# Performance work log

Measured on AMD Instinct MI355X. Metric: run time of the kernel, lower is better.

## Reference

```python
import jax, jax.numpy as jnp
import numpy as np

H = 8              # n_heads
N_PER_GRAPH = 64   # nodes per graph (equal-sized graphs)


def setup_inputs() -> dict:
    key = jax.random.key(0)
    ks = jax.random.split(key, 5)
    total, D = 65536, 512
    x = jax.random.normal(ks[0], (total, D), dtype=jnp.float32)
    batch = jnp.arange(total, dtype=jnp.int64) // N_PER_GRAPH  # sorted graph ids
    s = 1.0 / np.sqrt(D).astype(np.float32)
    # nn.MultiheadAttention packed in-proj (xavier-ish uniform) + zero bias
    in_proj_w = jax.random.uniform(ks[1], (3 * D, D), jnp.float32, -s, s)
    in_proj_b = jnp.zeros((3 * D,), jnp.float32)
    out_proj_w = jax.random.uniform(ks[2], (D, D), jnp.float32, -s, s)
    out_proj_b = jnp.zeros((D,), jnp.float32)
    gate_w = jax.random.uniform(ks[3], (1, D), jnp.float32, -s, s)
    gate_b = jnp.zeros((1,), jnp.float32)
    return {"x": x, "batch": batch, "in_proj_w": in_proj_w, "in_proj_b": in_proj_b,
            "out_proj_w": out_proj_w, "out_proj_b": out_proj_b,
            "gate_w": gate_w, "gate_b": gate_b}


def reference(x, batch, in_proj_w, in_proj_b, out_proj_w, out_proj_b, gate_w, gate_b):
    total, D = x.shape
    G = total // N_PER_GRAPH
    hd = D // H
    xg = x.reshape(G, N_PER_GRAPH, D)                       # [G, N, D]
    # packed qkv projection (torch: x @ in_proj_w.T + in_proj_b)
    qkv = jnp.einsum('gnd,ed->gne', xg, in_proj_w) + in_proj_b
    q, k, v = jnp.split(qkv, 3, axis=-1)
    def to_heads(t):
        return t.reshape(G, N_PER_GRAPH, H, hd).transpose(0, 2, 1, 3)  # [G, H, N, hd]
    q, k, v = to_heads(q), to_heads(k), to_heads(v)
    scores = jnp.einsum('ghnd,ghmd->ghnm', q, k) * (1.0 / np.sqrt(hd))
    attn = jax.nn.softmax(scores, axis=-1)
    ctx = jnp.einsum('ghnm,ghmd->ghnd', attn, v)
    ctx = ctx.transpose(0, 2, 1, 3).reshape(G, N_PER_GRAPH, D)
    attn_out = jnp.einsum('gnd,ed->gne', ctx, out_proj_w) + out_proj_b  # [G, N, D]
    gates = jax.nn.sigmoid(jnp.einsum('gnd,od->gno', attn_out, gate_w) + gate_b)
    return (attn_out * gates).sum(axis=1)                   # [G, D]
```

## Files before the change

kernel.cpp:

```cpp
#include <hip/hip_runtime.h>
#include <stdint.h>


typedef __attribute__((ext_vector_type(8))) short short8;
typedef __attribute__((ext_vector_type(4))) float f32x4;

#define D_ 512

#define WQKV_OFF   0u
#define WO_OFF     1572864u
#define UPART_OFF  2097152u
#define U_OFF      2129920u
#define C0_OFF     2131968u
#define SG_OFF     2132032u
#define WCTX_OFF   2136128u

__device__ __forceinline__ unsigned short f2bf(float f) {
    union { float f; unsigned int u; } t; t.f = f;
    unsigned int u = t.u;
    return (unsigned short)((u + 0x7FFFu + ((u >> 16) & 1u)) >> 16);
}
__device__ __forceinline__ unsigned pack2(float a, float b) {
    return (unsigned)f2bf(a) | ((unsigned)f2bf(b) << 16);
}

__global__ __launch_bounds__(256)
void convert_weights(const float* __restrict__ wqkv, const float* __restrict__ wo,
                     unsigned short* __restrict__ wbf) {
    const int i4 = blockIdx.x * 256 + threadIdx.x;
    float4 v;
    if (i4 < 196608) v = *(const float4*)(wqkv + (size_t)i4 * 4);
    else             v = *(const float4*)(wo   + (size_t)(i4 - 196608) * 4);
    uint2 p; p.x = pack2(v.x, v.y); p.y = pack2(v.z, v.w);
    *(uint2*)(wbf + (size_t)i4 * 4) = p;
}

__global__ __launch_bounds__(256)
void compute_u_partial(const float* __restrict__ wo, const float* __restrict__ gw,
                       float* __restrict__ upart) {
    const int b = blockIdx.x;
    const int t = threadIdx.x;
    float a0 = 0.f, a1 = 0.f;
    #pragma unroll 4
    for (int e = b * 32; e < b * 32 + 32; ++e) {
        const float ge = gw[e];
        a0 += wo[(size_t)e * 512 + t]       * ge;
        a1 += wo[(size_t)e * 512 + t + 256] * ge;
    }
    upart[b * 512 + t] = a0; upart[b * 512 + t + 256] = a1;
}

__global__ __launch_bounds__(256)
void finalize_u(const float* __restrict__ upart, const float* __restrict__ bo,
                const float* __restrict__ gw, const float* __restrict__ gb,
                float* __restrict__ u, float* __restrict__ c0) {
    const int t = threadIdx.x;
    float s0 = 0.f, s1 = 0.f;
    #pragma unroll
    for (int b = 0; b < 16; ++b) { s0 += upart[b*512 + t]; s1 += upart[b*512 + t + 256]; }
    u[t] = s0; u[t + 256] = s1;
    __shared__ float rb[256];
    rb[t] = bo[t] * gw[t] + bo[t + 256] * gw[t + 256];
    __syncthreads();
    for (int s = 128; s > 0; s >>= 1) { if (t < s) rb[t] += rb[t + s]; __syncthreads(); }
    if (t == 0) c0[0] = rb[0] + gb[0];
}

union U8 { unsigned u[4]; short8 s; };

__global__ __launch_bounds__(512, 2)
void attn_ctx_kernel(const float* __restrict__ x,
                     const unsigned short* __restrict__ wqkv,
                     const float* __restrict__ bqkv,
                     const float* __restrict__ u,
                     const float* __restrict__ c0,
                     unsigned short* __restrict__ wctx_ws,
                     float* __restrict__ sumgate)
{
    __shared__ unsigned short xs[64][520];
    __shared__ unsigned short scr[8][64][72];
    __shared__ float logitp[8][64];
    __shared__ float gatev[64];

    const int g    = blockIdx.x;
    const int tid  = threadIdx.x;
    const int w    = tid >> 6;
    const int lane = tid & 63;
    const int l15  = lane & 15;
    const int quad = lane >> 4;

    #pragma unroll
    for (int i = 0; i < 16; ++i) {
        int idx = tid + i * 512;
        int row = idx >> 7;
        int c4  = idx & 127;
        float4 v = *(const float4*)(x + ((size_t)(g*64 + row))*512 + c4*4);
        uint2 p; p.x = pack2(v.x, v.y); p.y = pack2(v.z, v.w);
        *(uint2*)(&xs[row][c4*4]) = p;
    }
    __syncthreads();

    const int h = w;
    unsigned short (*S)[72] = scr[w];

    U8 qA[4][2], kB[4][2];
    #pragma unroll
    for (int dt = 0; dt < 4; ++dt) {
        f32x4 aq[4], ak[4], av[4];
        #pragma unroll
        for (int nt = 0; nt < 4; ++nt) {
            aq[nt] = (f32x4){0.f,0.f,0.f,0.f};
            ak[nt] = (f32x4){0.f,0.f,0.f,0.f};
            av[nt] = (f32x4){0.f,0.f,0.f,0.f};
        }
        const unsigned short* wq = wqkv + (size_t)(          h*64 + dt*16 + l15) * 512;
        const unsigned short* wk = wqkv + (size_t)( 512 +    h*64 + dt*16 + l15) * 512;
        const unsigned short* wv = wqkv + (size_t)(1024 +    h*64 + dt*16 + l15) * 512;
        #pragma unroll 4
        for (int ks = 0; ks < 16; ++ks) {
            const int col = ks*32 + quad*8;
            short8 a0 = *(const short8*)(wq + col);
            short8 a1 = *(const short8*)(wk + col);
            short8 a2 = *(const short8*)(wv + col);
            #pragma unroll
            for (int nt = 0; nt < 4; ++nt) {
                short8 b = *(const short8*)(&xs[nt*16 + l15][col]);
                aq[nt] = __builtin_amdgcn_mfma_f32_16x16x32_bf16(a0, b, aq[nt], 0,0,0);
                ak[nt] = __builtin_amdgcn_mfma_f32_16x16x32_bf16(a1, b, ak[nt], 0,0,0);
                av[nt] = __builtin_amdgcn_mfma_f32_16x16x32_bf16(a2, b, av[nt], 0,0,0);
            }
        }
        float bq[4], bk2[4], bv2[4];
        #pragma unroll
        for (int r = 0; r < 4; ++r) {
            bq[r]  = bqkv[          h*64 + dt*16 + quad*4 + r];
            bk2[r] = bqkv[ 512 +    h*64 + dt*16 + quad*4 + r];
            bv2[r] = bqkv[1024 +    h*64 + dt*16 + quad*4 + r];
        }
        const bool take = ((quad >> 1) == (dt & 1));
        const int  ks2  = dt >> 1;
        #pragma unroll
        for (int nt = 0; nt < 4; ++nt) {
            unsigned q01 = pack2(aq[nt][0]+bq[0],  aq[nt][1]+bq[1]);
            unsigned q23 = pack2(aq[nt][2]+bq[2],  aq[nt][3]+bq[3]);
            unsigned k01 = pack2(ak[nt][0]+bk2[0], ak[nt][1]+bk2[1]);
            unsigned k23 = pack2(ak[nt][2]+bk2[2], ak[nt][3]+bk2[3]);
            #pragma unroll
            for (int j = 0; j < 4; ++j) {
                int srcl = ((quad & 1)*2 + (j >> 1))*16 + l15;
                unsigned tq = (unsigned)__shfl((int)((j & 1) ? q23 : q01), srcl);
                unsigned tk = (unsigned)__shfl((int)((j & 1) ? k23 : k01), srcl);
                if (take) { qA[nt][ks2].u[j] = tq; kB[nt][ks2].u[j] = tk; }
            }
            #pragma unroll
            for (int r = 0; r < 4; ++r)
                S[dt*16 + quad*4 + r][nt*16 + l15] = f2bf(av[nt][r] + bv2[r]);
        }
    }

    f32x4 sacc[4][4];
    #pragma unroll
    for (int a = 0; a < 4; ++a)
        #pragma unroll
        for (int b = 0; b < 4; ++b) sacc[a][b] = (f32x4){0.f,0.f,0.f,0.f};
    #pragma unroll
    for (int ks2 = 0; ks2 < 2; ++ks2)
        #pragma unroll
        for (int a = 0; a < 4; ++a)
            #pragma unroll
            for (int b = 0; b < 4; ++b)
                sacc[a][b] = __builtin_amdgcn_mfma_f32_16x16x32_bf16(
                                 qA[a][ks2].s, kB[b][ks2].s, sacc[a][b], 0,0,0);

    #pragma unroll
    for (int a = 0; a < 4; ++a) {
        #pragma unroll
        for (int r = 0; r < 4; ++r) {
            float m0 = -1e30f;
            #pragma unroll
            for (int b = 0; b < 4; ++b) { sacc[a][b][r] *= 0.125f; m0 = fmaxf(m0, sacc[a][b][r]); }
            m0 = fmaxf(m0, __shfl_xor(m0, 1));
            m0 = fmaxf(m0, __shfl_xor(m0, 2));
            m0 = fmaxf(m0, __shfl_xor(m0, 4));
            m0 = fmaxf(m0, __shfl_xor(m0, 8));
            float s = 0.f;
            #pragma unroll
            for (int b = 0; b < 4; ++b) { float e = __expf(sacc[a][b][r] - m0); sacc[a][b][r] = e; s += e; }
            s += __shfl_xor(s, 1); s += __shfl_xor(s, 2); s += __shfl_xor(s, 4); s += __shfl_xor(s, 8);
            float inv = 1.0f / s;
            #pragma unroll
            for (int b = 0; b < 4; ++b) sacc[a][b][r] *= inv;
        }
    }

    U8 vA[4][2];
    #pragma unroll
    for (int dtile = 0; dtile < 4; ++dtile)
        #pragma unroll
        for (int ks2 = 0; ks2 < 2; ++ks2)
            vA[dtile][ks2].s = *(const short8*)(&S[dtile*16 + l15][ks2*32 + quad*8]);

    #pragma unroll
    for (int a = 0; a < 4; ++a)
        #pragma unroll
        for (int b = 0; b < 4; ++b)
            #pragma unroll
            for (int r = 0; r < 4; ++r)
                S[a*16 + quad*4 + r][b*16 + l15] = f2bf(sacc[a][b][r]);

    U8 pB[4][2];
    #pragma unroll
    for (int a = 0; a < 4; ++a)
        #pragma unroll
        for (int ks2 = 0; ks2 < 2; ++ks2)
            pB[a][ks2].s = *(const short8*)(&S[a*16 + l15][ks2*32 + quad*8]);

    f32x4 cacc[4][4];
    #pragma unroll
    for (int dtile = 0; dtile < 4; ++dtile)
        #pragma unroll
        for (int a = 0; a < 4; ++a) cacc[dtile][a] = (f32x4){0.f,0.f,0.f,0.f};
    #pragma unroll
    for (int ks2 = 0; ks2 < 2; ++ks2)
        #pragma unroll
        for (int dtile = 0; dtile < 4; ++dtile)
            #pragma unroll
            for (int a = 0; a < 4; ++a)
                cacc[dtile][a] = __builtin_amdgcn_mfma_f32_16x16x32_bf16(
                                     vA[dtile][ks2].s, pB[a][ks2].s, cacc[dtile][a], 0,0,0);

    {
        float uv[4][4];
        #pragma unroll
        for (int dtile = 0; dtile < 4; ++dtile)
            #pragma unroll
            for (int r = 0; r < 4; ++r)
                uv[dtile][r] = u[h*64 + dtile*16 + quad*4 + r];
        #pragma unroll
        for (int a = 0; a < 4; ++a) {
            float s = 0.f;
            #pragma unroll
            for (int dtile = 0; dtile < 4; ++dtile)
                #pragma unroll
                for (int r = 0; r < 4; ++r)
                    s += cacc[dtile][a][r] * uv[dtile][r];
            s += __shfl_xor(s, 16); s += __shfl_xor(s, 32);
            if (quad == 0) logitp[w][a*16 + l15] = s;
        }
    }
    __syncthreads();

    if (tid < 64) {
        float lg = c0[0];
        #pragma unroll
        for (int ww = 0; ww < 8; ++ww) lg += logitp[ww][tid];
        float gt = 1.0f / (1.0f + __expf(-lg));
        gatev[tid] = gt;
        float s = gt;
        s += __shfl_xor(s, 1);  s += __shfl_xor(s, 2);  s += __shfl_xor(s, 4);
        s += __shfl_xor(s, 8);  s += __shfl_xor(s, 16); s += __shfl_xor(s, 32);
        if (tid == 0) sumgate[g] = s;
    }
    __syncthreads();

    {
        float gv[4];
        #pragma unroll
        for (int a = 0; a < 4; ++a) gv[a] = gatev[a*16 + l15];
        #pragma unroll
        for (int dtile = 0; dtile < 4; ++dtile) {
            float sr[4];
            #pragma unroll
            for (int r = 0; r < 4; ++r) {
                float s = cacc[dtile][0][r]*gv[0] + cacc[dtile][1][r]*gv[1]
                        + cacc[dtile][2][r]*gv[2] + cacc[dtile][3][r]*gv[3];
                s += __shfl_xor(s, 1); s += __shfl_xor(s, 2);
                s += __shfl_xor(s, 4); s += __shfl_xor(s, 8);
                sr[r] = s;
            }
            if (l15 == 0) {
                uint2 pk; pk.x = pack2(sr[0], sr[1]); pk.y = pack2(sr[2], sr[3]);
                *(uint2*)(wctx_ws + (size_t)g*512 + h*64 + dtile*16 + quad*4) = pk;
            }
        }
    }
}

__global__ __launch_bounds__(256, 4)
void outproj_kernel(const unsigned short* __restrict__ wo_bf,
                    const unsigned short* __restrict__ wctx_bf,
                    const float* __restrict__ bo,
                    const float* __restrict__ sumgate,
                    float* __restrict__ out)
{
    const int tid  = threadIdx.x;
    const int w    = tid >> 6;
    const int lane = tid & 63;
    const int l15  = lane & 15;
    const int quad = lane >> 4;
    const int g0   = blockIdx.x * 32;

    f32x4 oac[8][2];
    #pragma unroll
    for (int et = 0; et < 8; ++et)
        #pragma unroll
        for (int mt = 0; mt < 2; ++mt)
            oac[et][mt] = (f32x4){0.f,0.f,0.f,0.f};

    #pragma unroll 4
    for (int ks = 0; ks < 16; ++ks) {
        const int col = ks*32 + quad*8;
        short8 a0 = *(const short8*)(wctx_bf + (size_t)(g0 + l15)*D_      + col);
        short8 a1 = *(const short8*)(wctx_bf + (size_t)(g0 + 16 + l15)*D_ + col);
        #pragma unroll
        for (int et = 0; et < 8; ++et) {
            short8 b = *(const short8*)(wo_bf + (size_t)(w*128 + et*16 + l15)*D_ + col);
            oac[et][0] = __builtin_amdgcn_mfma_f32_16x16x32_bf16(a0, b, oac[et][0], 0,0,0);
            oac[et][1] = __builtin_amdgcn_mfma_f32_16x16x32_bf16(a1, b, oac[et][1], 0,0,0);
        }
    }
    #pragma unroll
    for (int et = 0; et < 8; ++et) {
        const int e = w*128 + et*16 + l15;
        const float bov = bo[e];
        #pragma unroll
        for (int mt = 0; mt < 2; ++mt)
            #pragma unroll
            for (int r = 0; r < 4; ++r) {
                const int gg = g0 + mt*16 + quad*4 + r;
                out[(size_t)gg*D_ + e] = oac[et][mt][r] + sumgate[gg] * bov;
            }
    }
}

extern "C" void kernel_launch(void* const* d_in, const int* in_sizes, int n_in,
                              void* d_out, int out_size, void* d_ws, size_t ws_size,
                              hipStream_t stream) {
    const float* x    = (const float*)d_in[0];
    const float* wqkv = (const float*)d_in[2];
    const float* bqkv = (const float*)d_in[3];
    const float* wo   = (const float*)d_in[4];
    const float* bo   = (const float*)d_in[5];
    const float* gw   = (const float*)d_in[6];
    const float* gb   = (const float*)d_in[7];
    float* out = (float*)d_out;

    char* ws = (char*)d_ws;
    unsigned short* wqkv_bf = (unsigned short*)(ws + WQKV_OFF);
    unsigned short* wo_bf   = (unsigned short*)(ws + WO_OFF);
    float*          upart   = (float*)(ws + UPART_OFF);
    float*          u_ws    = (float*)(ws + U_OFF);
    float*          c0_ws   = (float*)(ws + C0_OFF);
    float*          sg_ws   = (float*)(ws + SG_OFF);
    unsigned short* wctx_ws = (unsigned short*)(ws + WCTX_OFF);

    const int total = in_sizes[0] / D_;
    const int G     = total / 64;

    hipLaunchKernelGGL(convert_weights,   dim3(1024), dim3(256), 0, stream, wqkv, wo, wqkv_bf);
    hipLaunchKernelGGL(compute_u_partial, dim3(16),   dim3(256), 0, stream, wo, gw, upart);
    hipLaunchKernelGGL(finalize_u,        dim3(1),    dim3(256), 0, stream, upart, bo, gw, gb, u_ws, c0_ws);
    hipLaunchKernelGGL(attn_ctx_kernel,   dim3(G),    dim3(512), 0, stream,
                       x, wqkv_bf, bqkv, u_ws, c0_ws, wctx_ws, sg_ws);
    hipLaunchKernelGGL(outproj_kernel,    dim3(G/32), dim3(256), 0, stream,
                       wo_bf, wctx_ws, bo, sg_ws, out);
}
```

Measured before the change: 445.8 us.

## Reuse x LDS tile as scratch, defer V projection, raise occupancy, fuse prep kernels

Drops the separate per-wave scratch buffer (about 73 KB of LDS) and reuses the bf16 x tile as scratch after a barrier, with an XOR-swizzled layout to avoid bank conflicts. The V projection now runs after softmax, so V accumulators are not live alongside the Q/K accumulators. Launch bounds rise from 2 to 4 blocks per CU. The weight-conversion and u-partial prep kernels are merged into one launch. Freeing LDS and registers is meant to let more blocks run at once, at the cost of an extra barrier and a possibly tighter register budget that could spill.

```diff
diff --git a/kernel.cpp b/kernel.cpp
--- a/kernel.cpp
+++ b/kernel.cpp
@@ -23,31 +23,34 @@
 __device__ __forceinline__ unsigned pack2(float a, float b) {
     return (unsigned)f2bf(a) | ((unsigned)f2bf(b) << 16);
 }
+__device__ __forceinline__ int swz(int r, int m) {
+    return r*64 + ((((m >> 3) ^ (r & 7)) << 3) | (m & 7));
+}
 
 __global__ __launch_bounds__(256)
-void convert_weights(const float* __restrict__ wqkv, const float* __restrict__ wo,
-                     unsigned short* __restrict__ wbf) {
-    const int i4 = blockIdx.x * 256 + threadIdx.x;
-    float4 v;
-    if (i4 < 196608) v = *(const float4*)(wqkv + (size_t)i4 * 4);
-    else             v = *(const float4*)(wo   + (size_t)(i4 - 196608) * 4);
-    uint2 p; p.x = pack2(v.x, v.y); p.y = pack2(v.z, v.w);
-    *(uint2*)(wbf + (size_t)i4 * 4) = p;
-}
-
-__global__ __launch_bounds__(256)
-void compute_u_partial(const float* __restrict__ wo, const float* __restrict__ gw,
-                       float* __restrict__ upart) {
+void convert_and_u(const float* __restrict__ wqkv, const float* __restrict__ wo,
+                   const float* __restrict__ gw,
+                   unsigned short* __restrict__ wbf, float* __restrict__ upart) {
     const int b = blockIdx.x;
     const int t = threadIdx.x;
-    float a0 = 0.f, a1 = 0.f;
-    #pragma unroll 4
-    for (int e = b * 32; e < b * 32 + 32; ++e) {
-        const float ge = gw[e];
-        a0 += wo[(size_t)e * 512 + t]       * ge;
-        a1 += wo[(size_t)e * 512 + t + 256] * ge;
-    }
-    upart[b * 512 + t] = a0; upart[b * 512 + t + 256] = a1;
+    if (b < 1024) {
+        const int i4 = b * 256 + t;
+        float4 v;
+        if (i4 < 196608) v = *(const float4*)(wqkv + (size_t)i4 * 4);
+        else             v = *(const float4*)(wo   + (size_t)(i4 - 196608) * 4);
+        uint2 p; p.x = pack2(v.x, v.y); p.y = pack2(v.z, v.w);
+        *(uint2*)(wbf + (size_t)i4 * 4) = p;
+    } else {
+        const int bb = b - 1024;
+        float a0 = 0.f, a1 = 0.f;
+        #pragma unroll 4
+        for (int e = bb * 32; e < bb * 32 + 32; ++e) {
+            const float ge = gw[e];
+            a0 += wo[(size_t)e * 512 + t]       * ge;
+            a1 += wo[(size_t)e * 512 + t + 256] * ge;
+        }
+        upart[bb * 512 + t] = a0; upart[bb * 512 + t + 256] = a1;
+    }
 }
 
 __global__ __launch_bounds__(256)
@@ -68,7 +71,7 @@
 
 union U8 { unsigned u[4]; short8 s; };
 
-__global__ __launch_bounds__(512, 2)
+__global__ __launch_bounds__(512, 4)
 void attn_ctx_kernel(const float* __restrict__ x,
                      const unsigned short* __restrict__ wqkv,
                      const float* __restrict__ bqkv,
@@ -78,7 +81,6 @@
                      float* __restrict__ sumgate)
 {
     __shared__ unsigned short xs[64][520];
-    __shared__ unsigned short scr[8][64][72];
     __shared__ float logitp[8][64];
     __shared__ float gatev[64];
 
@@ -101,41 +103,35 @@
     __syncthreads();
 
     const int h = w;
-    unsigned short (*S)[72] = scr[w];
 
     U8 qA[4][2], kB[4][2];
     #pragma unroll
     for (int dt = 0; dt < 4; ++dt) {
-        f32x4 aq[4], ak[4], av[4];
+        f32x4 aq[4], ak[4];
         #pragma unroll
         for (int nt = 0; nt < 4; ++nt) {
             aq[nt] = (f32x4){0.f,0.f,0.f,0.f};
             ak[nt] = (f32x4){0.f,0.f,0.f,0.f};
-            av[nt] = (f32x4){0.f,0.f,0.f,0.f};
-        }
-        const unsigned short* wq = wqkv + (size_t)(          h*64 + dt*16 + l15) * 512;
-        const unsigned short* wk = wqkv + (size_t)( 512 +    h*64 + dt*16 + l15) * 512;
-        const unsigned short* wv = wqkv + (size_t)(1024 +    h*64 + dt*16 + l15) * 512;
+        }
+        const unsigned short* wq = wqkv + (size_t)(       h*64 + dt*16 + l15) * 512;
+        const unsigned short* wk = wqkv + (size_t)(512 +  h*64 + dt*16 + l15) * 512;
         #pragma unroll 4
         for (int ks = 0; ks < 16; ++ks) {
             const int col = ks*32 + quad*8;
             short8 a0 = *(const short8*)(wq + col);
             short8 a1 = *(const short8*)(wk + col);
-            short8 a2 = *(const short8*)(wv + col);
             #pragma unroll
             for (int nt = 0; nt < 4; ++nt) {
                 short8 b = *(const short8*)(&xs[nt*16 + l15][col]);
                 aq[nt] = __builtin_amdgcn_mfma_f32_16x16x32_bf16(a0, b, aq[nt], 0,0,0);
                 ak[nt] = __builtin_amdgcn_mfma_f32_16x16x32_bf16(a1, b, ak[nt], 0,0,0);
-                av[nt] = __builtin_amdgcn_mfma_f32_16x16x32_bf16(a2, b, av[nt], 0,0,0);
-            }
-        }
-        float bq[4], bk2[4], bv2[4];
+            }
+        }
+        float bq[4], bk2[4];
         #pragma unroll
         for (int r = 0; r < 4; ++r) {
-            bq[r]  = bqkv[          h*64 + dt*16 + quad*4 + r];
-            bk2[r] = bqkv[ 512 +    h*64 + dt*16 + quad*4 + r];
-            bv2[r] = bqkv[1024 +    h*64 + dt*16 + quad*4 + r];
+            bq[r]  = bqkv[       h*64 + dt*16 + quad*4 + r];
+            bk2[r] = bqkv[512 +  h*64 + dt*16 + quad*4 + r];
         }
         const bool take = ((quad >> 1) == (dt & 1));
         const int  ks2  = dt >> 1;
@@ -152,9 +148,6 @@
                 unsigned tk = (unsigned)__shfl((int)((j & 1) ? k23 : k01), srcl);
                 if (take) { qA[nt][ks2].u[j] = tq; kB[nt][ks2].u[j] = tk; }
             }
-            #pragma unroll
-            for (int r = 0; r < 4; ++r)
-                S[dt*16 + quad*4 + r][nt*16 + l15] = f2bf(av[nt][r] + bv2[r]);
         }
     }
 
@@ -192,28 +185,87 @@
             for (int b = 0; b < 4; ++b) sacc[a][b][r] *= inv;
         }
     }
-
+    unsigned ppk[4][4][2];
+    #pragma unroll
+    for (int a = 0; a < 4; ++a)
+        #pragma unroll
+        for (int b = 0; b < 4; ++b) {
+            ppk[a][b][0] = pack2(sacc[a][b][0], sacc[a][b][1]);
+            ppk[a][b][1] = pack2(sacc[a][b][2], sacc[a][b][3]);
+        }
+
+    unsigned avpk[4][4][2];
+    #pragma unroll
+    for (int dt = 0; dt < 4; ++dt) {
+        f32x4 av[4];
+        #pragma unroll
+        for (int nt = 0; nt < 4; ++nt) av[nt] = (f32x4){0.f,0.f,0.f,0.f};
+        const unsigned short* wv = wqkv + (size_t)(1024 + h*64 + dt*16 + l15) * 512;
+        #pragma unroll 4
+        for (int ks = 0; ks < 16; ++ks) {
+            const int col = ks*32 + quad*8;
+            short8 a2 = *(const short8*)(wv + col);
+            #pragma unroll
+            for (int nt = 0; nt < 4; ++nt) {
+                short8 b = *(const short8*)(&xs[nt*16 + l15][col]);
+                av[nt] = __builtin_amdgcn_mfma_f32_16x16x32_bf16(a2, b, av[nt], 0,0,0);
+            }
+        }
+        float bv2[4];
+        #pragma unroll
+        for (int r = 0; r < 4; ++r) bv2[r] = bqkv[1024 + h*64 + dt*16 + quad*4 + r];
+        #pragma unroll
+        for (int nt = 0; nt < 4; ++nt) {
+            avpk[dt][nt][0] = pack2(av[nt][0]+bv2[0], av[nt][1]+bv2[1]);
+            avpk[dt][nt][1] = pack2(av[nt][2]+bv2[2], av[nt][3]+bv2[3]);
+        }
+    }
+
+    __syncthreads();
+    unsigned short* S = ((unsigned short*)xs) + w*4096;
+
+    #pragma unroll
+    for (int dt = 0; dt < 4; ++dt)
+        #pragma unroll
+        for (int nt = 0; nt < 4; ++nt)
+            #pragma unroll
+            for (int p = 0; p < 2; ++p) {
+                unsigned uu = avpk[dt][nt][p];
+                int d = dt*16 + quad*4 + 2*p;
+                int m = nt*16 + l15;
+                S[swz(d,   m)] = (unsigned short)(uu & 0xFFFFu);
+                S[swz(d+1, m)] = (unsigned short)(uu >> 16);
+            }
     U8 vA[4][2];
     #pragma unroll
     for (int dtile = 0; dtile < 4; ++dtile)
         #pragma unroll
-        for (int ks2 = 0; ks2 < 2; ++ks2)
-            vA[dtile][ks2].s = *(const short8*)(&S[dtile*16 + l15][ks2*32 + quad*8]);
-
+        for (int ks2 = 0; ks2 < 2; ++ks2) {
+            int row = dtile*16 + l15;
+            int ch  = (ks2*4 + quad) ^ (row & 7);
+            vA[dtile][ks2].s = *(const short8*)(S + row*64 + ch*8);
+        }
     #pragma unroll
     for (int a = 0; a < 4; ++a)
         #pragma unroll
         for (int b = 0; b < 4; ++b)
             #pragma unroll
-            for (int r = 0; r < 4; ++r)
-                S[a*16 + quad*4 + r][b*16 + l15] = f2bf(sacc[a][b][r]);
-
+            for (int p = 0; p < 2; ++p) {
+                unsigned uu = ppk[a][b][p];
+                int n = a*16 + quad*4 + 2*p;
+                int m = b*16 + l15;
+                S[swz(n,   m)] = (unsigned short)(uu & 0xFFFFu);
+                S[swz(n+1, m)] = (unsigned short)(uu >> 16);
+            }
     U8 pB[4][2];
     #pragma unroll
     for (int a = 0; a < 4; ++a)
         #pragma unroll
-        for (int ks2 = 0; ks2 < 2; ++ks2)
-            pB[a][ks2].s = *(const short8*)(&S[a*16 + l15][ks2*32 + quad*8]);
+        for (int ks2 = 0; ks2 < 2; ++ks2) {
+            int row = a*16 + l15;
+            int ch  = (ks2*4 + quad) ^ (row & 7);
+            pB[a][ks2].s = *(const short8*)(S + row*64 + ch*8);
+        }
 
     f32x4 cacc[4][4];
     #pragma unroll
@@ -357,11 +409,12 @@
     const int total = in_sizes[0] / D_;
     const int G     = total / 64;
 
-    hipLaunchKernelGGL(convert_weights,   dim3(1024), dim3(256), 0, stream, wqkv, wo, wqkv_bf);
-    hipLaunchKernelGGL(compute_u_partial, dim3(16),   dim3(256), 0, stream, wo, gw, upart);
-    hipLaunchKernelGGL(finalize_u,        dim3(1),    dim3(256), 0, stream, upart, bo, gw, gb, u_ws, c0_ws);
-    hipLaunchKernelGGL(attn_ctx_kernel,   dim3(G),    dim3(512), 0, stream,
+    hipLaunchKernelGGL(convert_and_u, dim3(1040), dim3(256), 0, stream,
+                       wqkv, wo, gw, wqkv_bf, upart);
+    hipLaunchKernelGGL(finalize_u,    dim3(1),    dim3(256), 0, stream,
+                       upart, bo, gw, gb, u_ws, c0_ws);
+    hipLaunchKernelGGL(attn_ctx_kernel, dim3(G),  dim3(512), 0, stream,
                        x, wqkv_bf, bqkv, u_ws, c0_ws, wctx_ws, sg_ws);
-    hipLaunchKernelGGL(outproj_kernel,    dim3(G/32), dim3(256), 0, stream,
+    hipLaunchKernelGGL(outproj_kernel, dim3(G/32), dim3(256), 0, stream,
                        wo_bf, wctx_ws, bo, sg_ws, out);
 }
```

Result: slower. 505.2 us (+13.3%).
